# Kernel tuning notes

Measured on AMD Instinct MI355X. Metric: run time of the kernel, lower is better.

## Reference

```python
import jax, jax.numpy as jnp
import numpy as np

B, S, HID = 2, 2048, 4096
NH, NKV, D = 32, 8, 128
GROUPS = NH // NKV  # 4 query heads per KV head
THETA = 10000.0
MAX_SEQ = 4096


def _rope_tables():
    half = D // 2
    inv_freq = 1.0 / (THETA ** (np.arange(half, dtype=np.float32) / half))
    t = np.arange(MAX_SEQ, dtype=np.float32)
    freqs = np.outer(t, inv_freq)  # [MAX_SEQ, D//2]
    return jnp.asarray(np.cos(freqs)), jnp.asarray(np.sin(freqs))

ROPE_COS, ROPE_SIN = _rope_tables()


def _apply_rope(x, cos, sin):
    # x: [B, S, H, D]; cos/sin: [S, D//2]; half-split (NeoX) rotation as in _apply_rope_inline
    half = x.shape[-1] // 2
    x0, x1 = x[..., :half], x[..., half:]
    c = cos[None, :, None, :]
    s = sin[None, :, None, :]
    return jnp.concatenate([x0 * c - x1 * s, x0 * s + x1 * c], axis=-1)


def setup_inputs() -> dict:
    key = jax.random.key(0)
    ks = jax.random.split(key, 5)
    wscale = 1.0 / np.sqrt(HID).astype(np.float32)  # keep activations O(1)
    return {
        "x": jax.random.normal(ks[0], (B, S, HID), dtype=jnp.float32),
        "positions": jnp.arange(S, dtype=jnp.int32),
        "w_q": jax.random.normal(ks[1], (NH * D, HID), dtype=jnp.float32) * wscale,
        "w_k": jax.random.normal(ks[2], (NKV * D, HID), dtype=jnp.float32) * wscale,
        "w_v": jax.random.normal(ks[3], (NKV * D, HID), dtype=jnp.float32) * wscale,
        "w_o": jax.random.normal(ks[4], (HID, NH * D), dtype=jnp.float32) * wscale,
    }


def reference(x, positions, w_q, w_k, w_v, w_o):
    cos = ROPE_COS[positions]  # [S, D//2]
    sin = ROPE_SIN[positions]
    # Separate Q/K/V projections (no bias), as in the training forward()
    q = (x @ w_q.T).reshape(B, S, NH, D)
    k = (x @ w_k.T).reshape(B, S, NKV, D)
    v = (x @ w_v.T).reshape(B, S, NKV, D)
    q = _apply_rope(q, cos, sin)
    k = _apply_rope(k, cos, sin)
    # [B, H, S, D] layout
    q = q.transpose(0, 2, 1, 3)
    k = k.transpose(0, 2, 1, 3)
    v = v.transpose(0, 2, 1, 3)
    # GQA: group query heads over shared KV heads instead of repeating K/V
    qg = q.reshape(B, NKV, GROUPS, S, D)
    scale = 1.0 / jnp.sqrt(jnp.float32(D))
    scores = jnp.einsum("bkgqd,bkmd->bkgqm", qg, k) * scale  # [B, NKV, G, Sq, Skv]
    causal = jnp.tril(jnp.ones((S, S), dtype=bool))
    scores = jnp.where(causal[None, None, None], scores, jnp.float32(-jnp.inf))
    probs = jax.nn.softmax(scores, axis=-1)
    ctx = jnp.einsum("bkgqm,bkmd->bkgqd", probs, v)  # [B, NKV, G, S, D]
    ctx = ctx.reshape(B, NH, S, D).transpose(0, 2, 1, 3).reshape(B, S, NH * D)
    return ctx @ w_o.T
```

## Files before the change

kernel.cpp:

```cpp
#include <hip/hip_runtime.h>
#include <math.h>

typedef short s16x8 __attribute__((ext_vector_type(8)));
typedef float f32x4 __attribute__((ext_vector_type(4)));
typedef unsigned u32x4 __attribute__((ext_vector_type(4)));
typedef unsigned short u16;

#define S_LEN 2048
#define HID_DIM 4096
#define NH_Q 32
#define NKV_H 8
#define DHEAD 128

__device__ __forceinline__ u16 f2bf(float f) {
  unsigned u = __builtin_bit_cast(unsigned, f);
  u += 0x7fffu + ((u >> 16) & 1u);
  return (u16)(u >> 16);
}

__device__ __forceinline__ void gload16(const u16* g, u16* l) {
  __builtin_amdgcn_global_load_lds(
      (const __attribute__((address_space(1))) void*)g,
      (__attribute__((address_space(3))) void*)l, 16, 0, 0);
}

__global__ void cvt_kernel(const float* __restrict__ in, u16* __restrict__ out, int n4) {
  int stride = gridDim.x * blockDim.x;
  for (int i = blockIdx.x * blockDim.x + threadIdx.x; i < n4; i += stride) {
    float4 f = ((const float4*)in)[i];
    uint2 o;
    o.x = (unsigned)f2bf(f.x) | ((unsigned)f2bf(f.y) << 16);
    o.y = (unsigned)f2bf(f.z) | ((unsigned)f2bf(f.w) << 16);
    ((uint2*)out)[i] = o;
  }
}

__global__ void rope_table_kernel(const int* __restrict__ positions,
                                  float* __restrict__ cos_t, float* __restrict__ sin_t) {
  int idx = blockIdx.x * 256 + threadIdx.x;
  if (idx >= S_LEN * 64) return;
  int s = idx >> 6, j = idx & 63;
  float pos = (float)positions[s];
  float inv = expf(-(float)j * (9.210340371976184f / 64.0f));
  float ang = pos * inv;
  float sv, cv;
  sincosf(ang, &sv, &cv);
  cos_t[idx] = cv;
  sin_t[idx] = sv;
}

template<int EPI>
__global__ __launch_bounds__(512, 2) void gemm8ph_kernel(
    const u16* __restrict__ A, const u16* __restrict__ B,
    void* __restrict__ outp, int M, int N, int K,
    const float* __restrict__ cos_t, const float* __restrict__ sin_t) {
  __shared__ u16 LDS[65536];
  const int t = threadIdx.x;
  const int wave = t >> 6, lane = t & 63;
  const int l15 = lane & 15, lhi = lane >> 4;
  const int wr = wave >> 2, wc = wave & 3;
  const int gx = gridDim.x;
  const int nwg = gx * gridDim.y;
  const int id = blockIdx.y * gx + blockIdx.x;
  const int swz = (id & 7) * (nwg >> 3) + (id >> 3);
  const int bm = (swz / gx) * 256, bn = (swz % gx) * 256;

  const int sw = l15 & 7;
  int aoff[4][2], boff[2][2];
#pragma unroll
  for (int q = 0; q < 4; ++q)
#pragma unroll
    for (int ks = 0; ks < 2; ++ks)
      aoff[q][ks] = (wr * 64 + q * 16 + l15) * 64 + (((ks << 2) + lhi) ^ sw) * 8;
#pragma unroll
  for (int f = 0; f < 2; ++f)
#pragma unroll
    for (int ks = 0; ks < 2; ++ks)
      boff[f][ks] = (f * 64 + wc * 16 + l15) * 64 + (((ks << 2) + lhi) ^ sw) * 8;

  const int lr1 = t >> 3;
  const int cs1 = ((t & 7) ^ (lr1 & 7)) * 8;
  const int rA1 = lr1;
  const int rA2 = 128 + lr1;
  const int ldsw = wave * 512;

  const f32x4 fz = {0.f, 0.f, 0.f, 0.f};
  f32x4 acc[8][4];
#pragma unroll
  for (int mf = 0; mf < 8; ++mf)
#pragma unroll
    for (int nf = 0; nf < 4; ++nf) acc[mf][nf] = fz;

  auto stageA = [&](int tile, int h, int buf) {
    const size_t kb = (size_t)tile * 64;
    gload16(A + (size_t)(bm + h * 64 + rA1) * K + kb + cs1,
            &LDS[buf * 16384 + h * 8192 + ldsw]);
    gload16(A + (size_t)(bm + h * 64 + rA2) * K + kb + cs1,
            &LDS[buf * 16384 + h * 8192 + 4096 + ldsw]);
  };
  auto stageB = [&](int tile, int h, int buf) {
    const size_t kb = (size_t)tile * 64;
    gload16(B + (size_t)(bn + h * 128 + lr1) * K + kb + cs1,
            &LDS[32768 + buf * 16384 + h * 8192 + ldsw]);
    gload16(B + (size_t)(bn + h * 128 + 64 + lr1) * K + kb + cs1,
            &LDS[32768 + buf * 16384 + h * 8192 + 4096 + ldsw]);
  };

  s16x8 afr[4][2], bfr[2][2];
  auto readA = [&](int mfH, int buf) {
    const int base = buf * 16384 + mfH * 8192;
#pragma unroll
    for (int q = 0; q < 4; ++q)
#pragma unroll
      for (int ks = 0; ks < 2; ++ks)
        afr[q][ks] = *(const s16x8*)&LDS[base + aoff[q][ks]];
  };
  auto readB = [&](int nfH, int buf) {
    const int base = 32768 + buf * 16384 + nfH * 8192;
#pragma unroll
    for (int f = 0; f < 2; ++f)
#pragma unroll
      for (int ks = 0; ks < 2; ++ks)
        bfr[f][ks] = *(const s16x8*)&LDS[base + boff[f][ks]];
  };
  auto mfma16 = [&](int mfH, int nfH) {
    __builtin_amdgcn_s_setprio(1);
#pragma unroll
    for (int q = 0; q < 4; ++q)
#pragma unroll
      for (int f = 0; f < 2; ++f)
#pragma unroll
        for (int ks = 0; ks < 2; ++ks)
          acc[mfH * 4 + q][nfH * 2 + f] = __builtin_amdgcn_mfma_f32_16x16x32_bf16(
              afr[q][ks], bfr[f][ks], acc[mfH * 4 + q][nfH * 2 + f], 0, 0, 0);
    __builtin_amdgcn_s_setprio(0);
  };

#define PHASE_SYNC()                        \
  do {                                      \
    __builtin_amdgcn_s_barrier();           \
    asm volatile("s_waitcnt lgkmcnt(0)");   \
    __builtin_amdgcn_sched_barrier(0);      \
  } while (0)

  stageA(0, 0, 0); stageB(0, 0, 0); stageA(0, 1, 0); stageB(0, 1, 0);
  stageA(1, 0, 1); stageB(1, 1, 1);
  asm volatile("s_waitcnt vmcnt(4)");
  __builtin_amdgcn_sched_barrier(0);
  __builtin_amdgcn_s_barrier();

  const int nt = K >> 6;
  for (int i = 0; i < (nt >> 1); ++i) {
    const int t1 = 2 * i + 1, t2 = 2 * i + 2, t3 = 2 * i + 3;
    const bool s2 = t2 < nt, s3 = t3 < nt;
    readA(0, 0); readB(0, 0); stageA(t1, 1, 1);
    PHASE_SYNC(); mfma16(0, 0); __builtin_amdgcn_s_barrier();
    readB(1, 0); stageB(t1, 0, 1);
    PHASE_SYNC(); mfma16(0, 1); __builtin_amdgcn_s_barrier();
    readA(1, 0); if (s2) stageA(t2, 0, 0);
    PHASE_SYNC(); mfma16(1, 1); __builtin_amdgcn_s_barrier();
    readB(0, 0); if (s2) stageB(t2, 1, 0);
    if (s2) { asm volatile("s_waitcnt vmcnt(4)"); }
    else    { asm volatile("s_waitcnt vmcnt(0)"); }
    PHASE_SYNC(); mfma16(1, 0); __builtin_amdgcn_s_barrier();
    readA(0, 1); readB(0, 1); if (s2) stageA(t2, 1, 0);
    PHASE_SYNC(); mfma16(0, 0); __builtin_amdgcn_s_barrier();
    readB(1, 1); if (s2) stageB(t2, 0, 0);
    PHASE_SYNC(); mfma16(0, 1); __builtin_amdgcn_s_barrier();
    readA(1, 1); if (s3) stageA(t3, 0, 1);
    PHASE_SYNC(); mfma16(1, 1); __builtin_amdgcn_s_barrier();
    readB(0, 1); if (s3) stageB(t3, 1, 1);
    if (s3) { asm volatile("s_waitcnt vmcnt(4)"); }
    else    { asm volatile("s_waitcnt vmcnt(0)"); }
    PHASE_SYNC(); mfma16(1, 0); __builtin_amdgcn_s_barrier();
  }
#undef PHASE_SYNC

  if constexpr (EPI == 0) {
    float* C = (float*)outp;
#pragma unroll
    for (int mf = 0; mf < 8; ++mf) {
      int rb = bm + wr * 128 + mf * 16 + lhi * 4;
#pragma unroll
      for (int nfi = 0; nfi < 4; ++nfi) {
        int col = bn + wc * 16 + (nfi & 1) * 64 + (nfi >> 1) * 128 + l15;
#pragma unroll
        for (int i = 0; i < 4; ++i) C[(size_t)(rb + i) * N + col] = acc[mf][nfi][i];
      }
    }
  } else {
    u16* qp = (u16*)outp;
    u16* kp = qp + 16777216;
    u16* vp = kp + 4194304;
    if (bn < 5120) {
      const bool isQ = bn < 4096;
      u16* O = isQ ? qp : kp;
      const int hb = isQ ? (bn >> 7) : ((bn - 4096) >> 7);
      const int Hh = isQ ? NH_Q : NKV_H;
      const int j = wc * 16 + l15;
#pragma unroll
      for (int mf = 0; mf < 8; ++mf) {
        int rb = bm + wr * 128 + mf * 16 + lhi * 4;
#pragma unroll
        for (int p = 0; p < 2; ++p) {
          int head = hb + p;
#pragma unroll
          for (int i = 0; i < 4; ++i) {
            int m = rb + i;
            int b = m >> 11, srw = m & 2047;
            float c = cos_t[srw * 64 + j];
            float s = sin_t[srw * 64 + j];
            float x0 = acc[mf][2 * p][i];
            float x1 = acc[mf][2 * p + 1][i];
            size_t base = ((size_t)(b * Hh + head) * S_LEN + srw) * DHEAD;
            O[base + j] = f2bf(x0 * c - x1 * s);
            O[base + j + 64] = f2bf(x0 * s + x1 * c);
          }
        }
      }
    } else {
#pragma unroll
      for (int mf = 0; mf < 8; ++mf) {
        int rb = bm + wr * 128 + mf * 16 + lhi * 4;
#pragma unroll
        for (int nfi = 0; nfi < 4; ++nfi) {
          int colrel = bn - 5120 + wc * 16 + (nfi & 1) * 64 + (nfi >> 1) * 128 + l15;
          int head = colrel >> 7, d = colrel & 127;
#pragma unroll
          for (int i = 0; i < 4; ++i) {
            int m = rb + i;
            int b = m >> 11, srw = m & 2047;
            vp[((size_t)(b * NKV_H + head) * DHEAD + d) * S_LEN + srw] = f2bf(acc[mf][nfi][i]);
          }
        }
      }
    }
  }
}

template<int EPI, bool ABF16, bool BBF16>
__global__ __launch_bounds__(256) void gemm_kernel(
    const void* __restrict__ Aptr, const void* __restrict__ Bptr,
    void* __restrict__ outp, void* __restrict__ outp2, int M, int N, int K,
    const float* __restrict__ cos_t, const float* __restrict__ sin_t, int Hh) {
  __shared__ u16 As[128][72];
  __shared__ u16 Bs[128][72];
  const int t = threadIdx.x;
  const int wave = t >> 6, lane = t & 63;
  const int l15 = lane & 15, lhi = lane >> 4;
  const int gx = gridDim.x;
  const int nwg = gx * gridDim.y;
  const int id = blockIdx.y * gx + blockIdx.x;
  const int swz = (id & 7) * (nwg >> 3) + (id >> 3);
  const int bm = (swz / gx) * 128, bn = (swz % gx) * 128;

  const f32x4 fz = {0.f, 0.f, 0.f, 0.f};
  f32x4 acc[2][8];
#pragma unroll
  for (int a0 = 0; a0 < 2; ++a0)
#pragma unroll
    for (int b0 = 0; b0 < 8; ++b0) acc[a0][b0] = fz;

  for (int kt = 0; kt < K; kt += 64) {
    __syncthreads();
    if (ABF16) {
      const u16* A = (const u16*)Aptr;
#pragma unroll
      for (int p = 0; p < 4; ++p) {
        int row = p * 32 + (t >> 3), kc = (t & 7) * 8;
        *(s16x8*)&As[row][kc] = *(const s16x8*)(A + (size_t)(bm + row) * K + kt + kc);
      }
    } else {
      const float* A = (const float*)Aptr;
#pragma unroll
      for (int p = 0; p < 8; ++p) {
        int row = p * 16 + (t >> 4), kc = (t & 15) * 4;
        float4 f = *(const float4*)(A + (size_t)(bm + row) * K + kt + kc);
        unsigned* dst = (unsigned*)&As[row][kc];
        dst[0] = (unsigned)f2bf(f.x) | ((unsigned)f2bf(f.y) << 16);
        dst[1] = (unsigned)f2bf(f.z) | ((unsigned)f2bf(f.w) << 16);
      }
    }
    if (BBF16) {
      const u16* Bw = (const u16*)Bptr;
#pragma unroll
      for (int p = 0; p < 4; ++p) {
        int row = p * 32 + (t >> 3), kc = (t & 7) * 8;
        *(s16x8*)&Bs[row][kc] = *(const s16x8*)(Bw + (size_t)(bn + row) * K + kt + kc);
      }
    } else {
      const float* Bw = (const float*)Bptr;
#pragma unroll
      for (int p = 0; p < 8; ++p) {
        int row = p * 16 + (t >> 4), kc = (t & 15) * 4;
        float4 f = *(const float4*)(Bw + (size_t)(bn + row) * K + kt + kc);
        unsigned* dst = (unsigned*)&Bs[row][kc];
        dst[0] = (unsigned)f2bf(f.x) | ((unsigned)f2bf(f.y) << 16);
        dst[1] = (unsigned)f2bf(f.z) | ((unsigned)f2bf(f.w) << 16);
      }
    }
    __syncthreads();
#pragma unroll
    for (int ks = 0; ks < 2; ++ks) {
      s16x8 bfr[8];
#pragma unroll
      for (int nf = 0; nf < 8; ++nf)
        bfr[nf] = *(const s16x8*)&Bs[nf * 16 + l15][ks * 32 + lhi * 8];
#pragma unroll
      for (int mf = 0; mf < 2; ++mf) {
        s16x8 a = *(const s16x8*)&As[wave * 32 + mf * 16 + l15][ks * 32 + lhi * 8];
#pragma unroll
        for (int nf = 0; nf < 8; ++nf)
          acc[mf][nf] = __builtin_amdgcn_mfma_f32_16x16x32_bf16(a, bfr[nf], acc[mf][nf], 0, 0, 0);
      }
    }
  }

  if (EPI == 0) {
    float* C = (float*)outp;
#pragma unroll
    for (int mf = 0; mf < 2; ++mf)
#pragma unroll
      for (int nf = 0; nf < 8; ++nf) {
        int col = bn + nf * 16 + l15;
        int rb = bm + wave * 32 + mf * 16 + lhi * 4;
#pragma unroll
        for (int i = 0; i < 4; ++i) C[(size_t)(rb + i) * N + col] = acc[mf][nf][i];
      }
  } else if (EPI == 2) {
    u16* O = (u16*)outp;
    int h = bn >> 7;
#pragma unroll
    for (int mf = 0; mf < 2; ++mf)
#pragma unroll
      for (int nf = 0; nf < 4; ++nf) {
        int j = nf * 16 + l15;
        int rb = bm + wave * 32 + mf * 16 + lhi * 4;
#pragma unroll
        for (int i = 0; i < 4; ++i) {
          int m = rb + i;
          int b = m >> 11, srow = m & 2047;
          float c = cos_t[srow * 64 + j];
          float s = sin_t[srow * 64 + j];
          float x0 = acc[mf][nf][i];
          float x1 = acc[mf][nf + 4][i];
          size_t base = ((size_t)(b * Hh + h) * S_LEN + srow) * DHEAD;
          O[base + j] = f2bf(x0 * c - x1 * s);
          O[base + j + 64] = f2bf(x0 * s + x1 * c);
        }
      }
  } else {
    u16* O = (u16*)outp;
#pragma unroll
    for (int mf = 0; mf < 2; ++mf)
#pragma unroll
      for (int nf = 0; nf < 8; ++nf) {
        int col = bn + nf * 16 + l15;
        int h = col >> 7, d = col & 127;
        int rb = bm + wave * 32 + mf * 16 + lhi * 4;
#pragma unroll
        for (int i = 0; i < 4; ++i) {
          int m = rb + i;
          int b = m >> 11, srow = m & 2047;
          O[((size_t)(b * Hh + h) * DHEAD + d) * S_LEN + srow] = f2bf(acc[mf][nf][i]);
        }
      }
  }
}

#define KIDX(r, c) (((r) * 128 + (c)) ^ (((r) & 7) << 3))
#define VIDX(d, kv) (((d) * 64 + (kv)) ^ (((d) & 7) << 3))
__global__ __launch_bounds__(512) void attn_kernel(
    const u16* __restrict__ q, const u16* __restrict__ k, const u16* __restrict__ vt,
    u16* __restrict__ ctx) {
  __shared__ u16 Ks[64 * 128];
  __shared__ u16 Vts[128 * 64];

  const int t = threadIdx.x;
  const int wave = t >> 6, lane = t & 63;
  const int l15 = lane & 15, lhi = lane >> 4;
  const int pi = blockIdx.x, h = blockIdx.y, b = blockIdx.z;
  const int kvh = h >> 2;
  const int qsub[2] = {pi, 15 - pi};
  const int ntiles = 32 - 2 * pi;

  const u16* qb = q + ((size_t)(b * NH_Q + h)) * S_LEN * DHEAD;
  const u16* kb = k + ((size_t)(b * NKV_H + kvh)) * S_LEN * DHEAD;
  const u16* vtb = vt + ((size_t)(b * NKV_H + kvh)) * DHEAD * S_LEN;

  s16x8 qf[2][4];
#pragma unroll
  for (int s = 0; s < 2; ++s)
#pragma unroll
    for (int ks = 0; ks < 4; ++ks)
      qf[s][ks] = *(const s16x8*)(qb + (size_t)(qsub[s] * 128 + wave * 16 + l15) * DHEAD +
                                  ks * 32 + lhi * 8);

  const f32x4 fz = {0.f, 0.f, 0.f, 0.f};
  f32x4 acc[2][8];
#pragma unroll
  for (int s = 0; s < 2; ++s)
#pragma unroll
    for (int i = 0; i < 8; ++i) acc[s][i] = fz;
  float mrow[2] = {-INFINITY, -INFINITY};
  float lsum[2] = {0.f, 0.f};

  const float scale = 0.08838834764831845f;

  const int sl0 = l15 | (((2 * lhi) & 3) << 4);
  const int sl1 = sl0 | 16;
  const bool hisel = (lhi & 2) != 0;

  const int krow = t >> 3, kd0 = (t & 7) * 16;
  const int vrow = t >> 2, vk0 = (t & 3) * 16;
  s16x8 kr0, kr1, vr0, vr1;
  {
    const u16* p = kb + (size_t)krow * DHEAD + kd0;
    kr0 = *(const s16x8*)p;
    kr1 = *(const s16x8*)(p + 8);
    const u16* pv = vtb + (size_t)vrow * S_LEN + vk0;
    vr0 = *(const s16x8*)pv;
    vr1 = *(const s16x8*)(pv + 8);
  }

  for (int tt = 0; tt < ntiles; ++tt) {
    __syncthreads();
    *(s16x8*)&Ks[KIDX(krow, kd0)] = kr0;
    *(s16x8*)&Ks[KIDX(krow, kd0 + 8)] = kr1;
    *(s16x8*)&Vts[VIDX(vrow, vk0)] = vr0;
    *(s16x8*)&Vts[VIDX(vrow, vk0 + 8)] = vr1;
    __syncthreads();
    if (tt + 1 < ntiles) {
      const u16* p = kb + (size_t)((tt + 1) * 64 + krow) * DHEAD + kd0;
      kr0 = *(const s16x8*)p;
      kr1 = *(const s16x8*)(p + 8);
      const u16* pv = vtb + (size_t)vrow * S_LEN + (tt + 1) * 64 + vk0;
      vr0 = *(const s16x8*)pv;
      vr1 = *(const s16x8*)(pv + 8);
    }

    const int kc_base = tt * 64;
#pragma unroll
    for (int s = 0; s < 2; ++s) {
      const int wmin = qsub[s] * 128 + wave * 16;
      if (kc_base > wmin + 15) continue;
      f32x4 sacc[4];
#pragma unroll
      for (int i = 0; i < 4; ++i) sacc[i] = fz;
      __builtin_amdgcn_s_setprio(1);
#pragma unroll
      for (int ks = 0; ks < 4; ++ks) {
#pragma unroll
        for (int nf = 0; nf < 4; ++nf) {
          s16x8 kf = *(const s16x8*)&Ks[KIDX(nf * 16 + l15, ks * 32 + lhi * 8)];
          sacc[nf] = __builtin_amdgcn_mfma_f32_16x16x32_bf16(kf, qf[s][ks], sacc[nf], 0, 0, 0);
        }
      }
      __builtin_amdgcn_s_setprio(0);

      const int qg = wmin + l15;
      float pmax = -INFINITY;
      if (kc_base + 63 > wmin) {
#pragma unroll
        for (int nf = 0; nf < 4; ++nf)
#pragma unroll
          for (int i = 0; i < 4; ++i) {
            int kv = kc_base + nf * 16 + lhi * 4 + i;
            float sv = sacc[nf][i] * scale;
            sv = (kv <= qg) ? sv : -INFINITY;
            sacc[nf][i] = sv;
            pmax = fmaxf(pmax, sv);
          }
      } else {
#pragma unroll
        for (int nf = 0; nf < 4; ++nf)
#pragma unroll
          for (int i = 0; i < 4; ++i) {
            float sv = sacc[nf][i] * scale;
            sacc[nf][i] = sv;
            pmax = fmaxf(pmax, sv);
          }
      }
      pmax = fmaxf(pmax, __shfl_xor(pmax, 16, 64));
      pmax = fmaxf(pmax, __shfl_xor(pmax, 32, 64));

      if (!__all(pmax <= mrow[s] + 8.0f)) {
        float mnew = fmaxf(mrow[s], pmax);
        float alpha = __expf(mrow[s] - mnew);
        mrow[s] = mnew;
        lsum[s] *= alpha;
#pragma unroll
        for (int i = 0; i < 4; ++i) {
          float al = __shfl(alpha, (lane & 48) | (lhi * 4 + i), 64);
#pragma unroll
          for (int df = 0; df < 8; ++df) acc[s][df][i] *= al;
        }
      }

      float rsum = 0.f;
      unsigned pk[4][2];
#pragma unroll
      for (int nf = 0; nf < 4; ++nf) {
        float p0 = __expf(sacc[nf][0] - mrow[s]);
        float p1 = __expf(sacc[nf][1] - mrow[s]);
        float p2 = __expf(sacc[nf][2] - mrow[s]);
        float p3 = __expf(sacc[nf][3] - mrow[s]);
        rsum += (p0 + p1) + (p2 + p3);
        pk[nf][0] = (unsigned)f2bf(p0) | ((unsigned)f2bf(p1) << 16);
        pk[nf][1] = (unsigned)f2bf(p2) | ((unsigned)f2bf(p3) << 16);
      }
      rsum += __shfl_xor(rsum, 16, 64);
      rsum += __shfl_xor(rsum, 32, 64);
      lsum[s] += rsum;

      s16x8 pa[2];
#pragma unroll
      for (int ph = 0; ph < 2; ++ph) {
        unsigned lo0 = __shfl((int)pk[2 * ph][0], sl0, 64);
        unsigned hi0 = __shfl((int)pk[2 * ph + 1][0], sl0, 64);
        unsigned lo1 = __shfl((int)pk[2 * ph][1], sl0, 64);
        unsigned hi1 = __shfl((int)pk[2 * ph + 1][1], sl0, 64);
        unsigned lo2 = __shfl((int)pk[2 * ph][0], sl1, 64);
        unsigned hi2 = __shfl((int)pk[2 * ph + 1][0], sl1, 64);
        unsigned lo3 = __shfl((int)pk[2 * ph][1], sl1, 64);
        unsigned hi3 = __shfl((int)pk[2 * ph + 1][1], sl1, 64);
        u32x4 w;
        w[0] = hisel ? hi0 : lo0;
        w[1] = hisel ? hi1 : lo1;
        w[2] = hisel ? hi2 : lo2;
        w[3] = hisel ? hi3 : lo3;
        pa[ph] = __builtin_bit_cast(s16x8, w);
      }

      __builtin_amdgcn_s_setprio(1);
#pragma unroll
      for (int ph = 0; ph < 2; ++ph) {
#pragma unroll
        for (int df = 0; df < 8; ++df) {
          s16x8 bb = *(const s16x8*)&Vts[VIDX(df * 16 + l15, ph * 32 + lhi * 8)];
          acc[s][df] = __builtin_amdgcn_mfma_f32_16x16x32_bf16(pa[ph], bb, acc[s][df], 0, 0, 0);
        }
      }
      __builtin_amdgcn_s_setprio(0);
    }
  }

#pragma unroll
  for (int s = 0; s < 2; ++s) {
    float rl = 1.0f / lsum[s];
#pragma unroll
    for (int i = 0; i < 4; ++i) {
      float rli = __shfl(rl, (lane & 48) | (lhi * 4 + i), 64);
      int m = b * S_LEN + qsub[s] * 128 + wave * 16 + lhi * 4 + i;
#pragma unroll
      for (int df = 0; df < 8; ++df) {
        int col = h * DHEAD + df * 16 + l15;
        ctx[(size_t)m * (NH_Q * DHEAD) + col] = f2bf(acc[s][df][i] * rli);
      }
    }
  }
}

extern "C" void kernel_launch(void* const* d_in, const int* in_sizes, int n_in,
                              void* d_out, int out_size, void* d_ws, size_t ws_size,
                              hipStream_t stream) {
  const float* x = (const float*)d_in[0];
  const int* positions = (const int*)d_in[1];
  const float* wq = (const float*)d_in[2];
  const float* wk = (const float*)d_in[3];
  const float* wv = (const float*)d_in[4];
  const float* wo = (const float*)d_in[5];
  float* out = (float*)d_out;

  char* ws = (char*)d_ws;
  const size_t MB1 = 1048576;
  const size_t SZ_X = 33554432;
  const size_t SZ_WQKV = 50331648;
  const size_t SZ_Q = 33554432;
  const size_t SZ_WK = 8388608;
  const size_t NEED_FULL = MB1 + SZ_X + SZ_WQKV + SZ_Q + 2 * SZ_WK;

  float* cos_t = (float*)ws;
  float* sin_t = (float*)(ws + MB1 / 2);

  rope_table_kernel<<<512, 256, 0, stream>>>(positions, cos_t, sin_t);

  if (ws_size >= NEED_FULL) {
    char* p = ws + MB1;
    u16* x_bf = (u16*)p;    p += SZ_X;
    u16* wqkv_bf = (u16*)p; p += SZ_WQKV;
    u16* q_ws = (u16*)p;    p += SZ_Q;
    u16* k_ws = (u16*)p;    p += SZ_WK;
    u16* v_ws = (u16*)p;    p += SZ_WK;
    u16* ctx_ws = x_bf;

    cvt_kernel<<<2048, 256, 0, stream>>>(x, x_bf, 4194304);
    cvt_kernel<<<2048, 256, 0, stream>>>(wq, wqkv_bf, 4194304);
    cvt_kernel<<<1024, 256, 0, stream>>>(wk, wqkv_bf + 16777216, 1048576);
    cvt_kernel<<<1024, 256, 0, stream>>>(wv, wqkv_bf + 20971520, 1048576);

    gemm8ph_kernel<5><<<dim3(24, 16), 512, 0, stream>>>(
        x_bf, wqkv_bf, q_ws, 4096, 6144, 4096, cos_t, sin_t);
    cvt_kernel<<<2048, 256, 0, stream>>>(wo, wqkv_bf, 4194304);
    attn_kernel<<<dim3(8, 32, 2), 512, 0, stream>>>(q_ws, k_ws, v_ws, ctx_ws);
    gemm8ph_kernel<0><<<dim3(16, 16), 512, 0, stream>>>(
        ctx_ws, wqkv_bf, out, 4096, 4096, 4096, nullptr, nullptr);
  } else {
    u16* q_ws = (u16*)(ws + MB1);
    u16* k_ws = (u16*)(ws + MB1 + SZ_Q);
    u16* v_ws = (u16*)(ws + MB1 + SZ_Q + SZ_WK);
    u16* ctx_ws = (u16*)(ws + MB1 + SZ_Q + 2 * SZ_WK);

    gemm_kernel<2, false, false><<<dim3(32, 32), 256, 0, stream>>>(
        x, wq, q_ws, nullptr, 4096, 4096, 4096, cos_t, sin_t, NH_Q);
    gemm_kernel<2, false, false><<<dim3(8, 32), 256, 0, stream>>>(
        x, wk, k_ws, nullptr, 4096, 1024, 4096, cos_t, sin_t, NKV_H);
    gemm_kernel<4, false, false><<<dim3(8, 32), 256, 0, stream>>>(
        x, wv, v_ws, nullptr, 4096, 1024, 4096, nullptr, nullptr, NKV_H);
    attn_kernel<<<dim3(8, 32, 2), 512, 0, stream>>>(q_ws, k_ws, v_ws, ctx_ws);
    gemm_kernel<0, true, false><<<dim3(32, 32), 256, 0, stream>>>(
        ctx_ws, wo, out, nullptr, 4096, 4096, 4096, nullptr, nullptr, 0);
  }
}
```

Baseline: 540.6 us.

## Fuse fp32-to-bf16 conversions into one kernel and retune GEMM prefetch schedule

Replaces the separate conversion launches with a single kernel that converts x, wq, wk, wv and, when the workspace is large enough, wo into a dedicated buffer, cutting launch count and per-launch tail overhead. The 8-phase GEMM main loop is reordered: B fragments go into two register sets so B tiles for the next iteration can be staged earlier, with deeper vmcnt waits (6 loads in flight instead of 4). This costs extra VGPRs for the second B fragment set, and the larger-workspace path needs 32 MB more scratch.

```diff
diff --git a/kernel.cpp b/kernel.cpp
--- a/kernel.cpp
+++ b/kernel.cpp
@@ -32,6 +32,31 @@
     o.x = (unsigned)f2bf(f.x) | ((unsigned)f2bf(f.y) << 16);
     o.y = (unsigned)f2bf(f.z) | ((unsigned)f2bf(f.w) << 16);
     ((uint2*)out)[i] = o;
+  }
+}
+
+__global__ void cvt_all_kernel(const float* __restrict__ x, const float* __restrict__ wq,
+                               const float* __restrict__ wk, const float* __restrict__ wv,
+                               const float* __restrict__ wo, u16* __restrict__ x_bf,
+                               u16* __restrict__ wqkv_bf, u16* __restrict__ wo_bf,
+                               int with_wo) {
+  const int R0 = 4194304, R1 = 8388608, R2 = 9437184, R3 = 10485760, R4 = 14680064;
+  const int total = with_wo ? R4 : R3;
+  const int stride = gridDim.x * blockDim.x;
+  for (int i = blockIdx.x * blockDim.x + threadIdx.x; i < total; i += stride) {
+    const float* src;
+    u16* dst;
+    int off;
+    if (i < R0)      { src = x;  dst = x_bf;               off = i; }
+    else if (i < R1) { src = wq; dst = wqkv_bf;            off = i - R0; }
+    else if (i < R2) { src = wk; dst = wqkv_bf + 16777216; off = i - R1; }
+    else if (i < R3) { src = wv; dst = wqkv_bf + 20971520; off = i - R2; }
+    else             { src = wo; dst = wo_bf;              off = i - R3; }
+    float4 f = ((const float4*)src)[off];
+    uint2 o;
+    o.x = (unsigned)f2bf(f.x) | ((unsigned)f2bf(f.y) << 16);
+    o.y = (unsigned)f2bf(f.z) | ((unsigned)f2bf(f.w) << 16);
+    ((uint2*)dst)[off] = o;
   }
 }
 
@@ -106,7 +131,7 @@
             &LDS[32768 + buf * 16384 + h * 8192 + 4096 + ldsw]);
   };
 
-  s16x8 afr[4][2], bfr[2][2];
+  s16x8 afr[4][2], bfr[2][2], bfrK[2][2];
   auto readA = [&](int mfH, int buf) {
     const int base = buf * 16384 + mfH * 8192;
 #pragma unroll
@@ -115,15 +140,15 @@
       for (int ks = 0; ks < 2; ++ks)
         afr[q][ks] = *(const s16x8*)&LDS[base + aoff[q][ks]];
   };
-  auto readB = [&](int nfH, int buf) {
+  auto readB = [&](int nfH, int buf, s16x8 (&dst)[2][2]) {
     const int base = 32768 + buf * 16384 + nfH * 8192;
 #pragma unroll
     for (int f = 0; f < 2; ++f)
 #pragma unroll
       for (int ks = 0; ks < 2; ++ks)
-        bfr[f][ks] = *(const s16x8*)&LDS[base + boff[f][ks]];
+        dst[f][ks] = *(const s16x8*)&LDS[base + boff[f][ks]];
   };
-  auto mfma16 = [&](int mfH, int nfH) {
+  auto mfma16 = [&](int mfH, int nfH, const s16x8 (&bb)[2][2]) {
     __builtin_amdgcn_s_setprio(1);
 #pragma unroll
     for (int q = 0; q < 4; ++q)
@@ -132,7 +157,7 @@
 #pragma unroll
         for (int ks = 0; ks < 2; ++ks)
           acc[mfH * 4 + q][nfH * 2 + f] = __builtin_amdgcn_mfma_f32_16x16x32_bf16(
-              afr[q][ks], bfr[f][ks], acc[mfH * 4 + q][nfH * 2 + f], 0, 0, 0);
+              afr[q][ks], bb[f][ks], acc[mfH * 4 + q][nfH * 2 + f], 0, 0, 0);
     __builtin_amdgcn_s_setprio(0);
   };
 
@@ -143,36 +168,34 @@
     __builtin_amdgcn_sched_barrier(0);      \
   } while (0)
 
-  stageA(0, 0, 0); stageB(0, 0, 0); stageA(0, 1, 0); stageB(0, 1, 0);
-  stageA(1, 0, 1); stageB(1, 1, 1);
-  asm volatile("s_waitcnt vmcnt(4)");
+  stageA(0, 0, 0); stageB(0, 0, 0); stageB(0, 1, 0); stageA(0, 1, 0);
+  stageA(1, 0, 1); stageB(1, 0, 1); stageB(1, 1, 1);
+  asm volatile("s_waitcnt vmcnt(6)");
   __builtin_amdgcn_sched_barrier(0);
   __builtin_amdgcn_s_barrier();
 
   const int nt = K >> 6;
   for (int i = 0; i < (nt >> 1); ++i) {
-    const int t1 = 2 * i + 1, t2 = 2 * i + 2, t3 = 2 * i + 3;
-    const bool s2 = t2 < nt, s3 = t3 < nt;
-    readA(0, 0); readB(0, 0); stageA(t1, 1, 1);
-    PHASE_SYNC(); mfma16(0, 0); __builtin_amdgcn_s_barrier();
-    readB(1, 0); stageB(t1, 0, 1);
-    PHASE_SYNC(); mfma16(0, 1); __builtin_amdgcn_s_barrier();
-    readA(1, 0); if (s2) stageA(t2, 0, 0);
-    PHASE_SYNC(); mfma16(1, 1); __builtin_amdgcn_s_barrier();
-    readB(0, 0); if (s2) stageB(t2, 1, 0);
-    if (s2) { asm volatile("s_waitcnt vmcnt(4)"); }
+    const int u = 2 * i, v = 2 * i + 1;
+    const bool s2 = (u + 2) < nt;
+    readA(0, 0); readB(0, 0, bfrK); stageA(v, 1, 1);
+    PHASE_SYNC(); mfma16(0, 0, bfrK); __builtin_amdgcn_s_barrier();
+    readB(1, 0, bfr); if (s2) stageB(u + 2, 0, 0);
+    PHASE_SYNC(); mfma16(0, 1, bfr); __builtin_amdgcn_s_barrier();
+    readA(1, 0); if (s2) stageB(u + 2, 1, 0);
+    PHASE_SYNC(); mfma16(1, 1, bfr); __builtin_amdgcn_s_barrier();
+    if (s2) { stageA(u + 2, 0, 0); asm volatile("s_waitcnt vmcnt(6)"); }
     else    { asm volatile("s_waitcnt vmcnt(0)"); }
-    PHASE_SYNC(); mfma16(1, 0); __builtin_amdgcn_s_barrier();
-    readA(0, 1); readB(0, 1); if (s2) stageA(t2, 1, 0);
-    PHASE_SYNC(); mfma16(0, 0); __builtin_amdgcn_s_barrier();
-    readB(1, 1); if (s2) stageB(t2, 0, 0);
-    PHASE_SYNC(); mfma16(0, 1); __builtin_amdgcn_s_barrier();
-    readA(1, 1); if (s3) stageA(t3, 0, 1);
-    PHASE_SYNC(); mfma16(1, 1); __builtin_amdgcn_s_barrier();
-    readB(0, 1); if (s3) stageB(t3, 1, 1);
-    if (s3) { asm volatile("s_waitcnt vmcnt(4)"); }
+    PHASE_SYNC(); mfma16(1, 0, bfrK); __builtin_amdgcn_s_barrier();
+    readA(0, 1); readB(0, 1, bfrK); if (s2) stageA(u + 2, 1, 0);
+    PHASE_SYNC(); mfma16(0, 0, bfrK); __builtin_amdgcn_s_barrier();
+    readB(1, 1, bfr); if (s2) stageB(v + 2, 0, 1);
+    PHASE_SYNC(); mfma16(0, 1, bfr); __builtin_amdgcn_s_barrier();
+    readA(1, 1); if (s2) stageB(v + 2, 1, 1);
+    PHASE_SYNC(); mfma16(1, 1, bfr); __builtin_amdgcn_s_barrier();
+    if (s2) { stageA(v + 2, 0, 1); asm volatile("s_waitcnt vmcnt(6)"); }
     else    { asm volatile("s_waitcnt vmcnt(0)"); }
-    PHASE_SYNC(); mfma16(1, 0); __builtin_amdgcn_s_barrier();
+    PHASE_SYNC(); mfma16(1, 0, bfrK); __builtin_amdgcn_s_barrier();
   }
 #undef PHASE_SYNC
 
@@ -576,16 +599,34 @@
   const size_t MB1 = 1048576;
   const size_t SZ_X = 33554432;
   const size_t SZ_WQKV = 50331648;
+  const size_t SZ_WO = 33554432;
   const size_t SZ_Q = 33554432;
   const size_t SZ_WK = 8388608;
   const size_t NEED_FULL = MB1 + SZ_X + SZ_WQKV + SZ_Q + 2 * SZ_WK;
+  const size_t NEED_WO = NEED_FULL + SZ_WO;
 
   float* cos_t = (float*)ws;
   float* sin_t = (float*)(ws + MB1 / 2);
 
   rope_table_kernel<<<512, 256, 0, stream>>>(positions, cos_t, sin_t);
 
-  if (ws_size >= NEED_FULL) {
+  if (ws_size >= NEED_WO) {
+    char* p = ws + MB1;
+    u16* x_bf = (u16*)p;    p += SZ_X;
+    u16* wqkv_bf = (u16*)p; p += SZ_WQKV;
+    u16* wo_bf = (u16*)p;   p += SZ_WO;
+    u16* q_ws = (u16*)p;    p += SZ_Q;
+    u16* k_ws = (u16*)p;    p += SZ_WK;
+    u16* v_ws = (u16*)p;    p += SZ_WK;
+    u16* ctx_ws = x_bf;
+
+    cvt_all_kernel<<<2048, 256, 0, stream>>>(x, wq, wk, wv, wo, x_bf, wqkv_bf, wo_bf, 1);
+    gemm8ph_kernel<5><<<dim3(24, 16), 512, 0, stream>>>(
+        x_bf, wqkv_bf, q_ws, 4096, 6144, 4096, cos_t, sin_t);
+    attn_kernel<<<dim3(8, 32, 2), 512, 0, stream>>>(q_ws, k_ws, v_ws, ctx_ws);
+    gemm8ph_kernel<0><<<dim3(16, 16), 512, 0, stream>>>(
+        ctx_ws, wo_bf, out, 4096, 4096, 4096, nullptr, nullptr);
+  } else if (ws_size >= NEED_FULL) {
     char* p = ws + MB1;
     u16* x_bf = (u16*)p;    p += SZ_X;
     u16* wqkv_bf = (u16*)p; p += SZ_WQKV;
@@ -594,11 +635,7 @@
     u16* v_ws = (u16*)p;    p += SZ_WK;
     u16* ctx_ws = x_bf;
 
-    cvt_kernel<<<2048, 256, 0, stream>>>(x, x_bf, 4194304);
-    cvt_kernel<<<2048, 256, 0, stream>>>(wq, wqkv_bf, 4194304);
-    cvt_kernel<<<1024, 256, 0, stream>>>(wk, wqkv_bf + 16777216, 1048576);
-    cvt_kernel<<<1024, 256, 0, stream>>>(wv, wqkv_bf + 20971520, 1048576);
-
+    cvt_all_kernel<<<2048, 256, 0, stream>>>(x, wq, wk, wv, nullptr, x_bf, wqkv_bf, nullptr, 0);
     gemm8ph_kernel<5><<<dim3(24, 16), 512, 0, stream>>>(
         x_bf, wqkv_bf, q_ws, 4096, 6144, 4096, cos_t, sin_t);
     cvt_kernel<<<2048, 256, 0, stream>>>(wo, wqkv_bf, 4194304);
```

After: 537.1 us. Within noise of the previous version (-0.6%).
